# Kernel optimization log

Measured on AMD Instinct MI355X. Metric: run time of the kernel, lower is better.

## Reference

```python
import jax, jax.numpy as jnp
import numpy as np

E = 1024  # hidden_size
H = 16    # num_heads
D = E // H  # head_dim
LN_EPS = 1e-5


def setup_inputs() -> dict:
    key = jax.random.key(0)
    ks = jax.random.split(key, 7)
    B, S = 4, 2048
    scale = 1.0 / np.sqrt(E)
    return {
        "txt_emb": jax.random.normal(ks[0], (B, S, E), dtype=jnp.float32),
        "in_proj_w": jax.random.normal(ks[1], (3 * E, E), dtype=jnp.float32) * scale,
        "in_proj_b": jnp.zeros((3 * E,), dtype=jnp.float32),
        "out_proj_w": jax.random.normal(ks[2], (E, E), dtype=jnp.float32) * scale,
        "out_proj_b": jnp.zeros((E,), dtype=jnp.float32),
        "ln_gamma": jnp.ones((E,), dtype=jnp.float32),
        "ln_beta": jnp.zeros((E,), dtype=jnp.float32),
    }


def _layer_norm(x, gamma, beta):
    mu = jnp.mean(x, axis=-1, keepdims=True)
    var = jnp.var(x, axis=-1, keepdims=True)
    return (x - mu) * jax.lax.rsqrt(var + LN_EPS) * gamma + beta


def reference(txt_emb, in_proj_w, in_proj_b, out_proj_w, out_proj_b, ln_gamma, ln_beta):
    B, S, _ = txt_emb.shape
    # joint QKV projection (torch nn.MultiheadAttention semantics: x @ W.T + b)
    qkv = jnp.einsum('bse,fe->bsf', txt_emb, in_proj_w) + in_proj_b  # [B,S,3E]
    q, k, v = jnp.split(qkv, 3, axis=-1)
    # [B,H,S,D]
    q = q.reshape(B, S, H, D).transpose(0, 2, 1, 3)
    k = k.reshape(B, S, H, D).transpose(0, 2, 1, 3)
    v = v.reshape(B, S, H, D).transpose(0, 2, 1, 3)
    scores = jnp.einsum('bhqd,bhkd->bhqk', q, k) / np.sqrt(D)  # [B,H,S,S]
    causal = jnp.tril(jnp.ones((S, S), dtype=bool))
    scores = jnp.where(causal, scores, jnp.float32(-jnp.inf))
    attn = jax.nn.softmax(scores, axis=-1)
    ctx = jnp.einsum('bhqk,bhkd->bhqd', attn, v)  # [B,H,S,D]
    ctx = ctx.transpose(0, 2, 1, 3).reshape(B, S, E)
    attn_out = jnp.einsum('bse,fe->bsf', ctx, out_proj_w) + out_proj_b
    return _layer_norm(txt_emb + attn_out, ln_gamma, ln_beta)
```

## Files before the change

kernel.cpp:

```cpp
#include <hip/hip_runtime.h>
#include <hip/hip_bf16.h>
#include <stdint.h>

#define B_   4
#define S_   2048
#define E_   1024
#define H_   16
#define D_   64
#define M_   (B_ * S_)
#define E3_  (3 * E_)

#define QSCALE 0.18033688011112042f

typedef __bf16 bf16_t;
typedef bf16_t bf16x8 __attribute__((ext_vector_type(8)));
typedef float  f32x4  __attribute__((ext_vector_type(4)));
typedef float  f32x16 __attribute__((ext_vector_type(16)));

__device__ __forceinline__ ushort f2bf(float f) {
  union { float f; uint32_t u; } v; v.f = f;
  uint32_t r = v.u + 0x7fffu + ((v.u >> 16) & 1u);
  return (ushort)(r >> 16);
}

__device__ __forceinline__ unsigned cvtpk(float lo, float hi_) {
  unsigned d;
  asm("v_cvt_pk_bf16_f32 %0, %1, %2" : "=v"(d) : "v"(lo), "v"(hi_));
  return d;
}

__device__ __forceinline__ void gload_lds16(const void* g, void* l) {
  __builtin_amdgcn_global_load_lds((const __attribute__((address_space(1))) void*)g,
                                   (__attribute__((address_space(3))) void*)l,
                                   16, 0, 0);
}

__global__ __launch_bounds__(256) void cvt_f32_bf16(const float* __restrict__ in,
                                                    ushort* __restrict__ out, int n4,
                                                    int scale_row4, float scale) {
  int i = blockIdx.x * blockDim.x + threadIdx.x;
  if (i < n4) {
    float4 v = reinterpret_cast<const float4*>(in)[i];
    if (i < scale_row4) { v.x *= scale; v.y *= scale; v.z *= scale; v.w *= scale; }
    ushort4 o;
    o.x = f2bf(v.x); o.y = f2bf(v.y); o.z = f2bf(v.z); o.w = f2bf(v.w);
    reinterpret_cast<ushort4*>(out)[i] = o;
  }
}

template <int MODE>
__global__ __launch_bounds__(256) void gemm_bt2(const ushort* __restrict__ A,
                                                const ushort* __restrict__ Bt,
                                                const float* __restrict__ bias,
                                                void* __restrict__ out0,
                                                ushort* __restrict__ vTout,
                                                int Ndim, int K) {
  __shared__ __align__(16) char lds[3][16384];

  const int tid  = threadIdx.x;
  const int lane = tid & 63, wid = tid >> 6;
  const int w = wid;
  const int wr = wid >> 1, wc = wid & 1;

  const int nx  = Ndim >> 7;
  const int nwg = gridDim.x;
  const int b0  = blockIdx.x;
  const int nb  = (b0 & 7) * (nwg >> 3) + (b0 >> 3);
  const int bm  = (nb / nx) * 128, bn = (nb % nx) * 128;

  const int srow  = tid >> 2;
  const int sslot = (tid & 3) ^ (srow & 3) ^ ((srow >> 2) & 3);
  const ushort* aS = A  + (size_t)(bm + srow) * K + sslot * 8;
  const ushort* bS = Bt + (size_t)(bn + srow) * K + sslot * 8;

#define STAGE_A(T, BUF)                                                          \
  do {                                                                           \
    gload_lds16(aS + (size_t)(T) * 32,              (void*)((BUF) + w * 1024));  \
    gload_lds16(aS + (size_t)(T) * 32 + 64 * K,     (void*)((BUF) + 4096 + w * 1024)); \
  } while (0)
#define STAGE_B(T, BUF)                                                          \
  do {                                                                           \
    gload_lds16(bS + (size_t)(T) * 32,              (void*)((BUF) + 8192 + w * 1024)); \
    gload_lds16(bS + (size_t)(T) * 32 + 64 * K,     (void*)((BUF) + 12288 + w * 1024)); \
  } while (0)

  const int lr15 = lane & 15;
  const int ksub = lane >> 4;
  const int slot = (ksub ^ (lr15 & 3) ^ ((lr15 >> 2) & 3)) * 16;
  const int arow_b = (wr * 64 + lr15) * 64;
  const int brow_b = 8192 + (wc * 64 + lr15) * 64;

#define LDA4(BUF)                                                                \
  do {                                                                           \
    _Pragma("unroll")                                                            \
    for (int rb = 0; rb < 4; ++rb)                                               \
      af[rb] = *(const bf16x8*)((BUF) + arow_b + rb * 1024 + slot);              \
  } while (0)
#define LDB2(BUF, CB)                                                            \
  do {                                                                           \
    _Pragma("unroll")                                                            \
    for (int n = 0; n < 2; ++n)                                                  \
      bfr[n] = *(const bf16x8*)((BUF) + brow_b + ((CB) + n) * 1024 + slot);      \
  } while (0)
#define MFMA8(CB)                                                                \
  do {                                                                           \
    __builtin_amdgcn_s_setprio(1);                                               \
    _Pragma("unroll")                                                            \
    for (int rb = 0; rb < 4; ++rb)                                               \
      _Pragma("unroll")                                                          \
      for (int n = 0; n < 2; ++n)                                                \
        acc[rb][(CB) + n] = __builtin_amdgcn_mfma_f32_16x16x32_bf16(             \
            af[rb], bfr[n], acc[rb][(CB) + n], 0, 0, 0);                         \
    __builtin_amdgcn_s_setprio(0);                                               \
  } while (0)

  f32x4 acc[4][4] = {};
  bf16x8 af[4], bfr[2];

  char* buf0 = &lds[0][0];
  char* buf1 = &lds[1][0];
  char* buf2 = &lds[2][0];

  const int nt = K >> 5;

  STAGE_A(0, buf0); STAGE_B(0, buf0);
  STAGE_A(1, buf1); STAGE_B(1, buf1);
  asm volatile("s_waitcnt vmcnt(4)" ::: "memory");
  __builtin_amdgcn_s_barrier();
  __builtin_amdgcn_sched_barrier(0);

  for (int t = 0; t < nt; ++t) {
    if (t < nt - 2) STAGE_A(t + 2, buf2);
    LDA4(buf0);
    LDB2(buf0, 0);
    __builtin_amdgcn_s_barrier();
    asm volatile("s_waitcnt lgkmcnt(0)" ::: "memory");
    __builtin_amdgcn_sched_barrier(0);
    MFMA8(0);
    __builtin_amdgcn_s_barrier();
    __builtin_amdgcn_sched_barrier(0);
    if (t < nt - 2) STAGE_B(t + 2, buf2);
    LDB2(buf0, 2);
    __builtin_amdgcn_s_barrier();
    asm volatile("s_waitcnt lgkmcnt(0)" ::: "memory");
    __builtin_amdgcn_sched_barrier(0);
    MFMA8(2);
    if (t < nt - 2) asm volatile("s_waitcnt vmcnt(4)" ::: "memory");
    else if (t == nt - 2) asm volatile("s_waitcnt vmcnt(0)" ::: "memory");
    __builtin_amdgcn_s_barrier();
    __builtin_amdgcn_sched_barrier(0);
    char* tmp = buf0; buf0 = buf1; buf1 = buf2; buf2 = tmp;
  }

#pragma unroll
  for (int rb = 0; rb < 4; ++rb) {
#pragma unroll
    for (int cb = 0; cb < 4; ++cb) {
      const int col = bn + wc * 64 + cb * 16 + lr15;
      float bv = bias[col];
      if (MODE == 1 && col < 1024) bv *= QSCALE;
      const int row0 = bm + wr * 64 + rb * 16 + ksub * 4;
      if (MODE == 0) {
#pragma unroll
        for (int r = 0; r < 4; ++r)
          ((float*)out0)[(size_t)(row0 + r) * Ndim + col] = acc[rb][cb][r] + bv;
      } else {
        if (col < 2048) {
#pragma unroll
          for (int r = 0; r < 4; ++r)
            ((ushort*)out0)[(size_t)(row0 + r) * 2048 + col] = f2bf(acc[rb][cb][r] + bv);
        } else {
          ushort4 vv;
          vv.x = f2bf(acc[rb][cb][0] + bv);
          vv.y = f2bf(acc[rb][cb][1] + bv);
          vv.z = f2bf(acc[rb][cb][2] + bv);
          vv.w = f2bf(acc[rb][cb][3] + bv);
          const size_t vidx = ((size_t)((row0 >> 11) * 1024 + (col - 2048))) * 2048 + (row0 & 2047);
          *reinterpret_cast<ushort4*>(&vTout[vidx]) = vv;
        }
      }
    }
  }
#undef STAGE_A
#undef STAGE_B
#undef LDA4
#undef LDB2
#undef MFMA8
}

__global__ __launch_bounds__(512) void attn_causal(const ushort* __restrict__ qk,
                                                   const ushort* __restrict__ vT,
                                                   ushort* __restrict__ ctx) {
  __shared__ __align__(16) char lds[2][16384];

  const int tid = threadIdx.x;
  const int w = tid >> 6, lane = tid & 63;
  const int l31 = lane & 31, hi = lane >> 5;

  const int bid = blockIdx.x;
  const int bh = (bid & 7) * 8 + ((bid >> 3) & 7);
  const int g6 = bid >> 6;
  const int qb = (g6 < 4) ? (7 - g6) : (g6 - 4);
  const int b = bh >> 4, h = bh & 15;
  const int qbase = qb * 256;
  const int tmax = 4 * qb + 3;
  const int qw = qbase + w * 32;
  const int q_g = qw + l31;
  const int my_tmax = (qw + 31) >> 6;

  const ushort* qrow = qk + (size_t)(b * S_ + q_g) * 2048 + h * 64;
  bf16x8 qf[4];
#pragma unroll
  for (int st = 0; st < 4; ++st)
    qf[st] = *reinterpret_cast<const bf16x8*>(qrow + st * 16 + hi * 8);

  const int srow = tid >> 3;
  const int swz  = ((tid & 7) * 16) ^ ((srow & 7) << 4);
  const char* kbase = (const char*)qk + ((size_t)(b * S_ + srow) * 2048 + 1024 + h * 64) * 2 + swz;
  const char* vbase = (const char*)vT + ((size_t)(bh * 64 + srow) * 2048) * 2 + swz;

  f32x16 Ot0 = {}, Ot1 = {};
  float m_r = -__builtin_inff(), l_r = 0.f;

  const int kswz = ((l31 & 7) << 4);

#define STAGE(T, BUFI)                                                              \
  do {                                                                              \
    gload_lds16(kbase + (size_t)(T) * (64 * 2048 * 2), &lds[BUFI][w * 1024]);       \
    gload_lds16(vbase + (size_t)(T) * 128,             &lds[BUFI][8192 + w * 1024]);\
  } while (0)

  STAGE(0, 0);
  for (int t = 0; t <= tmax; ++t) {
    const int bufi = t & 1;
    if (t < tmax) {
      STAGE(t + 1, bufi ^ 1);
      asm volatile("s_waitcnt vmcnt(2)" ::: "memory");
    } else {
      asm volatile("s_waitcnt vmcnt(0)" ::: "memory");
    }
    __builtin_amdgcn_s_barrier();
    __builtin_amdgcn_sched_barrier(0);

    if (t <= my_tmax) {
      const char* Kt = &lds[bufi][0];
      const char* Vp = &lds[bufi][8192];

      f32x16 T0 = {}, T1 = {};
#pragma unroll
      for (int st = 0; st < 4; ++st) {
        const int cb = (st * 32 + hi * 16) ^ kswz;
        bf16x8 k0 = *(const bf16x8*)(Kt + l31 * 128 + cb);
        bf16x8 k1 = *(const bf16x8*)(Kt + (32 + l31) * 128 + cb);
        T0 = __builtin_amdgcn_mfma_f32_32x32x16_bf16(k0, qf[st], T0, 0, 0, 0);
        T1 = __builtin_amdgcn_mfma_f32_32x32x16_bf16(k1, qf[st], T1, 0, 0, 0);
      }

      float p[32];
      const bool needmask = (t * 64 + 63) > qw;
      const int kvb = t * 64 + 4 * hi;
#pragma unroll
      for (int g = 0; g < 4; ++g) {
#pragma unroll
        for (int j = 0; j < 4; ++j) {
          float v0 = T0[4 * g + j], v1 = T1[4 * g + j];
          if (needmask) {
            const int kv0 = kvb + 8 * g + j;
            v0 = (kv0      <= q_g) ? v0 : -__builtin_inff();
            v1 = (kv0 + 32 <= q_g) ? v1 : -__builtin_inff();
          }
          p[4 * g + j] = v0;
          p[16 + 4 * g + j] = v1;
        }
      }
      float pmax = p[0];
#pragma unroll
      for (int i = 1; i < 31; i += 2) pmax = fmaxf(fmaxf(pmax, p[i]), p[i + 1]);
      pmax = fmaxf(pmax, p[31]);
      pmax = fmaxf(pmax, __shfl_xor(pmax, 32));

      if (!__all(pmax - m_r <= 8.f)) {
        const float mn = fmaxf(m_r, pmax);
        const float sc = exp2f(m_r - mn);
        m_r = mn;
        l_r *= sc;
#pragma unroll
        for (int i = 0; i < 16; ++i) { Ot0[i] *= sc; Ot1[i] *= sc; }
      }
      float sum = 0.f;
#pragma unroll
      for (int i = 0; i < 32; ++i) { p[i] = exp2f(p[i] - m_r); sum += p[i]; }
      sum += __shfl_xor(sum, 32);
      l_r += sum;

#pragma unroll
      for (int ks = 0; ks < 4; ++ks) {
        const unsigned a = cvtpk(p[8 * ks + 0], p[8 * ks + 1]);
        const unsigned bq = cvtpk(p[8 * ks + 2], p[8 * ks + 3]);
        const unsigned c = cvtpk(p[8 * ks + 4], p[8 * ks + 5]);
        const unsigned d = cvtpk(p[8 * ks + 6], p[8 * ks + 7]);
        const unsigned x = hi ? a : c;
        const unsigned y = hi ? bq : d;
        const unsigned xp = (unsigned)__shfl_xor((int)x, 32);
        const unsigned yp = (unsigned)__shfl_xor((int)y, 32);
        union { unsigned u[4]; bf16x8 v; } pa;
        pa.u[0] = hi ? xp : a;
        pa.u[1] = hi ? yp : bq;
        pa.u[2] = hi ? c : xp;
        pa.u[3] = hi ? d : yp;
        const int cb = (ks * 32 + hi * 16) ^ kswz;
        bf16x8 v0 = *(const bf16x8*)(Vp + l31 * 128 + cb);
        bf16x8 v1 = *(const bf16x8*)(Vp + (32 + l31) * 128 + cb);
        Ot0 = __builtin_amdgcn_mfma_f32_32x32x16_bf16(v0, pa.v, Ot0, 0, 0, 0);
        Ot1 = __builtin_amdgcn_mfma_f32_32x32x16_bf16(v1, pa.v, Ot1, 0, 0, 0);
      }
    }
    __builtin_amdgcn_s_barrier();
    __builtin_amdgcn_sched_barrier(0);
  }

  const float inv = 1.0f / l_r;
  ushort* crow = ctx + (size_t)(b * S_ + q_g) * 1024 + h * 64;
#pragma unroll
  for (int g = 0; g < 4; ++g) {
#pragma unroll
    for (int jp = 0; jp < 2; ++jp) {
      const int d0 = 2 * jp + 8 * g + 4 * hi;
      const int r = 4 * g + 2 * jp;
      *(unsigned*)(crow + d0)      = cvtpk(Ot0[r] * inv, Ot0[r + 1] * inv);
      *(unsigned*)(crow + 32 + d0) = cvtpk(Ot1[r] * inv, Ot1[r + 1] * inv);
    }
  }
#undef STAGE
}

__global__ __launch_bounds__(256) void resid_ln(const float* __restrict__ x,
                                                const float* __restrict__ ao,
                                                const float* __restrict__ gamma,
                                                const float* __restrict__ beta,
                                                float* __restrict__ out) {
  const int row = blockIdx.x;
  const int tid = threadIdx.x;
  const size_t base = (size_t)row * E_;

  float4 xv = reinterpret_cast<const float4*>(x + base)[tid];
  float4 av = reinterpret_cast<const float4*>(ao + base)[tid];
  const float v0 = xv.x + av.x, v1 = xv.y + av.y, v2 = xv.z + av.z, v3 = xv.w + av.w;
  float s  = v0 + v1 + v2 + v3;
  float s2 = v0 * v0 + v1 * v1 + v2 * v2 + v3 * v3;
#pragma unroll
  for (int off = 32; off >= 1; off >>= 1) {
    s  += __shfl_xor(s, off);
    s2 += __shfl_xor(s2, off);
  }
  __shared__ float red[8];
  const int wid = tid >> 6, lane = tid & 63;
  if (lane == 0) { red[wid] = s; red[4 + wid] = s2; }
  __syncthreads();
  s  = red[0] + red[1] + red[2] + red[3];
  s2 = red[4] + red[5] + red[6] + red[7];
  const float mu  = s * (1.f / E_);
  const float var = s2 * (1.f / E_) - mu * mu;
  const float rsd = rsqrtf(var + 1e-5f);

  float4 gv = reinterpret_cast<const float4*>(gamma)[tid];
  float4 bv = reinterpret_cast<const float4*>(beta)[tid];
  float4 ov;
  ov.x = (v0 - mu) * rsd * gv.x + bv.x;
  ov.y = (v1 - mu) * rsd * gv.y + bv.y;
  ov.z = (v2 - mu) * rsd * gv.z + bv.z;
  ov.w = (v3 - mu) * rsd * gv.w + bv.w;
  reinterpret_cast<float4*>(out + base)[tid] = ov;
}

extern "C" void kernel_launch(void* const* d_in, const int* in_sizes, int n_in,
                              void* d_out, int out_size, void* d_ws, size_t ws_size,
                              hipStream_t stream) {
  (void)in_sizes; (void)n_in; (void)out_size; (void)ws_size;
  const float* x     = (const float*)d_in[0];
  const float* w_in  = (const float*)d_in[1];
  const float* b_in  = (const float*)d_in[2];
  const float* w_out = (const float*)d_in[3];
  const float* b_out = (const float*)d_in[4];
  const float* gamma = (const float*)d_in[5];
  const float* beta  = (const float*)d_in[6];
  float* out = (float*)d_out;

  char* ws = (char*)d_ws;
  ushort* xb    = (ushort*)(ws);
  ushort* winb  = (ushort*)(ws + 16777216);
  ushort* woutb = (ushort*)(ws + 23068672);
  ushort* qkb   = (ushort*)(ws + 25165824);
  ushort* vTb   = (ushort*)(ws + 58720256);
  ushort* ctxb  = (ushort*)(ws + 75497472);
  float*  ao    = (float*)(ws + 92274688);

  cvt_f32_bf16<<<dim3((M_ * E_) / 4 / 256), 256, 0, stream>>>(x, xb, (M_ * E_) / 4, 0, 1.f);
  cvt_f32_bf16<<<dim3((E3_ * E_) / 4 / 256), 256, 0, stream>>>(w_in, winb, (E3_ * E_) / 4,
                                                               (E_ * E_) / 4, QSCALE);
  cvt_f32_bf16<<<dim3((E_ * E_) / 4 / 256), 256, 0, stream>>>(w_out, woutb, (E_ * E_) / 4, 0, 1.f);

  gemm_bt2<1><<<dim3(1536), 256, 0, stream>>>(xb, winb, b_in, qkb, vTb, E3_, E_);
  attn_causal<<<dim3(512), 512, 0, stream>>>(qkb, vTb, ctxb);
  gemm_bt2<0><<<dim3(512), 256, 0, stream>>>(ctxb, woutb, b_out, ao, nullptr, E_, E_);
  resid_ln<<<dim3(M_), 256, 0, stream>>>(x, ao, gamma, beta, out);
}
```

Before: 202.1 us.

## Merge conversion kernels, store out-proj in bf16, and double attention KV tile per stage

Replaces the three f32-to-bf16 conversion launches with one grid-stride kernel. The output-projection GEMM now writes bf16 instead of f32, which halves the intermediate traffic read back by the residual LayerNorm kernel. The attention kernel stages two 64-key K/V tiles per barrier with doubled LDS, which halves the number of barrier/wait points. These cut launch overhead and memory traffic, at the cost of more LDS per block and extra bf16 rounding of the attention output before the residual add.

Result: faster. 192.3 us (-4.9%).

```diff
diff --git a/kernel.cpp b/kernel.cpp
--- a/kernel.cpp
+++ b/kernel.cpp
@@ -23,6 +23,11 @@
   return (ushort)(r >> 16);
 }
 
+__device__ __forceinline__ float bf2f(ushort u) {
+  union { uint32_t u; float f; } v; v.u = ((uint32_t)u) << 16;
+  return v.f;
+}
+
 __device__ __forceinline__ unsigned cvtpk(float lo, float hi_) {
   unsigned d;
   asm("v_cvt_pk_bf16_f32 %0, %1, %2" : "=v"(d) : "v"(lo), "v"(hi_));
@@ -35,16 +40,22 @@
                                    16, 0, 0);
 }
 
-__global__ __launch_bounds__(256) void cvt_f32_bf16(const float* __restrict__ in,
-                                                    ushort* __restrict__ out, int n4,
-                                                    int scale_row4, float scale) {
-  int i = blockIdx.x * blockDim.x + threadIdx.x;
-  if (i < n4) {
-    float4 v = reinterpret_cast<const float4*>(in)[i];
-    if (i < scale_row4) { v.x *= scale; v.y *= scale; v.z *= scale; v.w *= scale; }
+__global__ __launch_bounds__(256) void cvt_all(const float* __restrict__ x,
+                                               const float* __restrict__ w_in,
+                                               const float* __restrict__ w_out,
+                                               ushort* __restrict__ xb,
+                                               ushort* __restrict__ winb,
+                                               ushort* __restrict__ woutb) {
+  const int stride = gridDim.x * blockDim.x;
+  for (int i = blockIdx.x * blockDim.x + threadIdx.x; i < 3145728; i += stride) {
+    const float* src; ushort* dst; int j; float sc = 1.f;
+    if (i < 2097152)      { src = x;     dst = xb;    j = i; }
+    else if (i < 2883584) { src = w_in;  dst = winb;  j = i - 2097152; if (j < 262144) sc = QSCALE; }
+    else                  { src = w_out; dst = woutb; j = i - 2883584; }
+    float4 v = reinterpret_cast<const float4*>(src)[j];
     ushort4 o;
-    o.x = f2bf(v.x); o.y = f2bf(v.y); o.z = f2bf(v.z); o.w = f2bf(v.w);
-    reinterpret_cast<ushort4*>(out)[i] = o;
+    o.x = f2bf(v.x * sc); o.y = f2bf(v.y * sc); o.z = f2bf(v.z * sc); o.w = f2bf(v.w * sc);
+    reinterpret_cast<ushort4*>(dst)[j] = o;
   }
 }
 
@@ -163,7 +174,7 @@
       if (MODE == 0) {
 #pragma unroll
         for (int r = 0; r < 4; ++r)
-          ((float*)out0)[(size_t)(row0 + r) * Ndim + col] = acc[rb][cb][r] + bv;
+          ((ushort*)out0)[(size_t)(row0 + r) * Ndim + col] = f2bf(acc[rb][cb][r] + bv);
       } else {
         if (col < 2048) {
 #pragma unroll
@@ -191,7 +202,7 @@
 __global__ __launch_bounds__(512) void attn_causal(const ushort* __restrict__ qk,
                                                    const ushort* __restrict__ vT,
                                                    ushort* __restrict__ ctx) {
-  __shared__ __align__(16) char lds[2][16384];
+  __shared__ __align__(16) char lds[2][32768];
 
   const int tid = threadIdx.x;
   const int w = tid >> 6, lane = tid & 63;
@@ -202,11 +213,10 @@
   const int g6 = bid >> 6;
   const int qb = (g6 < 4) ? (7 - g6) : (g6 - 4);
   const int b = bh >> 4, h = bh & 15;
-  const int qbase = qb * 256;
-  const int tmax = 4 * qb + 3;
-  const int qw = qbase + w * 32;
+  const int qw = qb * 256 + w * 32;
   const int q_g = qw + l31;
   const int my_tmax = (qw + 31) >> 6;
+  const int U = 2 * qb + 2;
 
   const ushort* qrow = qk + (size_t)(b * S_ + q_g) * 2048 + h * 64;
   bf16x8 qf[4];
@@ -224,95 +234,102 @@
 
   const int kswz = ((l31 & 7) << 4);
 
-#define STAGE(T, BUFI)                                                              \
-  do {                                                                              \
-    gload_lds16(kbase + (size_t)(T) * (64 * 2048 * 2), &lds[BUFI][w * 1024]);       \
-    gload_lds16(vbase + (size_t)(T) * 128,             &lds[BUFI][8192 + w * 1024]);\
-  } while (0)
-
-  STAGE(0, 0);
-  for (int t = 0; t <= tmax; ++t) {
-    const int bufi = t & 1;
-    if (t < tmax) {
-      STAGE(t + 1, bufi ^ 1);
-      asm volatile("s_waitcnt vmcnt(2)" ::: "memory");
+#define STAGE_PAIR(U2, BUFI)                                                            \
+  do {                                                                                  \
+    const size_t t0_ = (size_t)(U2) * 2;                                                \
+    gload_lds16(kbase + t0_ * 262144,          &lds[BUFI][w * 1024]);                   \
+    gload_lds16(kbase + (t0_ + 1) * 262144,    &lds[BUFI][8192 + w * 1024]);            \
+    gload_lds16(vbase + t0_ * 128,             &lds[BUFI][16384 + w * 1024]);           \
+    gload_lds16(vbase + t0_ * 128 + 128,       &lds[BUFI][24576 + w * 1024]);           \
+  } while (0)
+
+  STAGE_PAIR(0, 0);
+  for (int u = 0; u < U; ++u) {
+    const int bufi = u & 1;
+    if (u < U - 1) {
+      STAGE_PAIR(u + 1, bufi ^ 1);
+      asm volatile("s_waitcnt vmcnt(4)" ::: "memory");
     } else {
       asm volatile("s_waitcnt vmcnt(0)" ::: "memory");
     }
     __builtin_amdgcn_s_barrier();
     __builtin_amdgcn_sched_barrier(0);
 
-    if (t <= my_tmax) {
-      const char* Kt = &lds[bufi][0];
-      const char* Vp = &lds[bufi][8192];
-
-      f32x16 T0 = {}, T1 = {};
-#pragma unroll
-      for (int st = 0; st < 4; ++st) {
-        const int cb = (st * 32 + hi * 16) ^ kswz;
-        bf16x8 k0 = *(const bf16x8*)(Kt + l31 * 128 + cb);
-        bf16x8 k1 = *(const bf16x8*)(Kt + (32 + l31) * 128 + cb);
-        T0 = __builtin_amdgcn_mfma_f32_32x32x16_bf16(k0, qf[st], T0, 0, 0, 0);
-        T1 = __builtin_amdgcn_mfma_f32_32x32x16_bf16(k1, qf[st], T1, 0, 0, 0);
-      }
-
-      float p[32];
-      const bool needmask = (t * 64 + 63) > qw;
-      const int kvb = t * 64 + 4 * hi;
-#pragma unroll
-      for (int g = 0; g < 4; ++g) {
-#pragma unroll
-        for (int j = 0; j < 4; ++j) {
-          float v0 = T0[4 * g + j], v1 = T1[4 * g + j];
-          if (needmask) {
-            const int kv0 = kvb + 8 * g + j;
-            v0 = (kv0      <= q_g) ? v0 : -__builtin_inff();
-            v1 = (kv0 + 32 <= q_g) ? v1 : -__builtin_inff();
+#pragma unroll
+    for (int s = 0; s < 2; ++s) {
+      const int t = 2 * u + s;
+      if (t <= my_tmax) {
+        const char* Kt = &lds[bufi][s * 8192];
+        const char* Vp = &lds[bufi][16384 + s * 8192];
+
+        f32x16 T0 = {}, T1 = {};
+#pragma unroll
+        for (int st = 0; st < 4; ++st) {
+          const int cb = (st * 32 + hi * 16) ^ kswz;
+          bf16x8 k0 = *(const bf16x8*)(Kt + l31 * 128 + cb);
+          bf16x8 k1 = *(const bf16x8*)(Kt + (32 + l31) * 128 + cb);
+          T0 = __builtin_amdgcn_mfma_f32_32x32x16_bf16(k0, qf[st], T0, 0, 0, 0);
+          T1 = __builtin_amdgcn_mfma_f32_32x32x16_bf16(k1, qf[st], T1, 0, 0, 0);
+        }
+
+        float p[32];
+        const bool needmask = (t * 64 + 63) > qw;
+        const int kvb = t * 64 + 4 * hi;
+#pragma unroll
+        for (int g = 0; g < 4; ++g) {
+#pragma unroll
+          for (int j = 0; j < 4; ++j) {
+            float v0 = T0[4 * g + j], v1 = T1[4 * g + j];
+            if (needmask) {
+              const int kv0 = kvb + 8 * g + j;
+              v0 = (kv0      <= q_g) ? v0 : -__builtin_inff();
+              v1 = (kv0 + 32 <= q_g) ? v1 : -__builtin_inff();
+            }
+            p[4 * g + j] = v0;
+            p[16 + 4 * g + j] = v1;
           }
-          p[4 * g + j] = v0;
-          p[16 + 4 * g + j] = v1;
         }
-      }
-      float pmax = p[0];
-#pragma unroll
-      for (int i = 1; i < 31; i += 2) pmax = fmaxf(fmaxf(pmax, p[i]), p[i + 1]);
-      pmax = fmaxf(pmax, p[31]);
-      pmax = fmaxf(pmax, __shfl_xor(pmax, 32));
-
-      if (!__all(pmax - m_r <= 8.f)) {
-        const float mn = fmaxf(m_r, pmax);
-        const float sc = exp2f(m_r - mn);
-        m_r = mn;
-        l_r *= sc;
-#pragma unroll
-        for (int i = 0; i < 16; ++i) { Ot0[i] *= sc; Ot1[i] *= sc; }
-      }
-      float sum = 0.f;
-#pragma unroll
-      for (int i = 0; i < 32; ++i) { p[i] = exp2f(p[i] - m_r); sum += p[i]; }
-      sum += __shfl_xor(sum, 32);
-      l_r += sum;
-
-#pragma unroll
-      for (int ks = 0; ks < 4; ++ks) {
-        const unsigned a = cvtpk(p[8 * ks + 0], p[8 * ks + 1]);
-        const unsigned bq = cvtpk(p[8 * ks + 2], p[8 * ks + 3]);
-        const unsigned c = cvtpk(p[8 * ks + 4], p[8 * ks + 5]);
-        const unsigned d = cvtpk(p[8 * ks + 6], p[8 * ks + 7]);
-        const unsigned x = hi ? a : c;
-        const unsigned y = hi ? bq : d;
-        const unsigned xp = (unsigned)__shfl_xor((int)x, 32);
-        const unsigned yp = (unsigned)__shfl_xor((int)y, 32);
-        union { unsigned u[4]; bf16x8 v; } pa;
-        pa.u[0] = hi ? xp : a;
-        pa.u[1] = hi ? yp : bq;
-        pa.u[2] = hi ? c : xp;
-        pa.u[3] = hi ? d : yp;
-        const int cb = (ks * 32 + hi * 16) ^ kswz;
-        bf16x8 v0 = *(const bf16x8*)(Vp + l31 * 128 + cb);
-        bf16x8 v1 = *(const bf16x8*)(Vp + (32 + l31) * 128 + cb);
-        Ot0 = __builtin_amdgcn_mfma_f32_32x32x16_bf16(v0, pa.v, Ot0, 0, 0, 0);
-        Ot1 = __builtin_amdgcn_mfma_f32_32x32x16_bf16(v1, pa.v, Ot1, 0, 0, 0);
+        float pmax = p[0];
+#pragma unroll
+        for (int i = 1; i < 31; i += 2) pmax = fmaxf(fmaxf(pmax, p[i]), p[i + 1]);
+        pmax = fmaxf(pmax, p[31]);
+        pmax = fmaxf(pmax, __shfl_xor(pmax, 32));
+
+        if (!__all(pmax - m_r <= 8.f)) {
+          const float mn = fmaxf(m_r, pmax);
+          const float sc = exp2f(m_r - mn);
+          m_r = mn;
+          l_r *= sc;
+#pragma unroll
+          for (int i = 0; i < 16; ++i) { Ot0[i] *= sc; Ot1[i] *= sc; }
+        }
+        float sum = 0.f;
+#pragma unroll
+        for (int i = 0; i < 32; ++i) { p[i] = exp2f(p[i] - m_r); sum += p[i]; }
+        sum += __shfl_xor(sum, 32);
+        l_r += sum;
+
+#pragma unroll
+        for (int ks = 0; ks < 4; ++ks) {
+          const unsigned a = cvtpk(p[8 * ks + 0], p[8 * ks + 1]);
+          const unsigned bq = cvtpk(p[8 * ks + 2], p[8 * ks + 3]);
+          const unsigned c = cvtpk(p[8 * ks + 4], p[8 * ks + 5]);
+          const unsigned d = cvtpk(p[8 * ks + 6], p[8 * ks + 7]);
+          const unsigned x = hi ? a : c;
+          const unsigned y = hi ? bq : d;
+          const unsigned xp = (unsigned)__shfl_xor((int)x, 32);
+          const unsigned yp = (unsigned)__shfl_xor((int)y, 32);
+          union { unsigned u[4]; bf16x8 v; } pa;
+          pa.u[0] = hi ? xp : a;
+          pa.u[1] = hi ? yp : bq;
+          pa.u[2] = hi ? c : xp;
+          pa.u[3] = hi ? d : yp;
+          const int cb = (ks * 32 + hi * 16) ^ kswz;
+          bf16x8 v0 = *(const bf16x8*)(Vp + l31 * 128 + cb);
+          bf16x8 v1 = *(const bf16x8*)(Vp + (32 + l31) * 128 + cb);
+          Ot0 = __builtin_amdgcn_mfma_f32_32x32x16_bf16(v0, pa.v, Ot0, 0, 0, 0);
+          Ot1 = __builtin_amdgcn_mfma_f32_32x32x16_bf16(v1, pa.v, Ot1, 0, 0, 0);
+        }
       }
     }
     __builtin_amdgcn_s_barrier();
@@ -331,11 +348,11 @@
       *(unsigned*)(crow + 32 + d0) = cvtpk(Ot1[r] * inv, Ot1[r + 1] * inv);
     }
   }
-#undef STAGE
+#undef STAGE_PAIR
 }
 
 __global__ __launch_bounds__(256) void resid_ln(const float* __restrict__ x,
-                                                const float* __restrict__ ao,
+                                                const ushort* __restrict__ ao,
                                                 const float* __restrict__ gamma,
                                                 const float* __restrict__ beta,
                                                 float* __restrict__ out) {
@@ -344,8 +361,9 @@
   const size_t base = (size_t)row * E_;
 
   float4 xv = reinterpret_cast<const float4*>(x + base)[tid];
-  float4 av = reinterpret_cast<const float4*>(ao + base)[tid];
-  const float v0 = xv.x + av.x, v1 = xv.y + av.y, v2 = xv.z + av.z, v3 = xv.w + av.w;
+  ushort4 au = reinterpret_cast<const ushort4*>(ao + base)[tid];
+  const float v0 = xv.x + bf2f(au.x), v1 = xv.y + bf2f(au.y);
+  const float v2 = xv.z + bf2f(au.z), v3 = xv.w + bf2f(au.w);
   float s  = v0 + v1 + v2 + v3;
   float s2 = v0 * v0 + v1 * v1 + v2 * v2 + v3 * v3;
 #pragma unroll
@@ -393,15 +411,12 @@
   ushort* qkb   = (ushort*)(ws + 25165824);
   ushort* vTb   = (ushort*)(ws + 58720256);
   ushort* ctxb  = (ushort*)(ws + 75497472);
-  float*  ao    = (float*)(ws + 92274688);
-
-  cvt_f32_bf16<<<dim3((M_ * E_) / 4 / 256), 256, 0, stream>>>(x, xb, (M_ * E_) / 4, 0, 1.f);
-  cvt_f32_bf16<<<dim3((E3_ * E_) / 4 / 256), 256, 0, stream>>>(w_in, winb, (E3_ * E_) / 4,
-                                                               (E_ * E_) / 4, QSCALE);
-  cvt_f32_bf16<<<dim3((E_ * E_) / 4 / 256), 256, 0, stream>>>(w_out, woutb, (E_ * E_) / 4, 0, 1.f);
+  ushort* aob   = (ushort*)(ws + 92274688);
+
+  cvt_all<<<dim3(2048), 256, 0, stream>>>(x, w_in, w_out, xb, winb, woutb);
 
   gemm_bt2<1><<<dim3(1536), 256, 0, stream>>>(xb, winb, b_in, qkb, vTb, E3_, E_);
   attn_causal<<<dim3(512), 512, 0, stream>>>(qkb, vTb, ctxb);
-  gemm_bt2<0><<<dim3(512), 256, 0, stream>>>(ctxb, woutb, b_out, ao, nullptr, E_, E_);
-  resid_ln<<<dim3(M_), 256, 0, stream>>>(x, ao, gamma, beta, out);
-}
+  gemm_bt2<0><<<dim3(512), 256, 0, stream>>>(ctxb, woutb, b_out, aob, nullptr, E_, E_);
+  resid_ln<<<dim3(M_), 256, 0, stream>>>(x, aob, gamma, beta, out);
+}
```
